# Kernel optimization log

Hardware: AMD Instinct MI355X
Metric: run time of the kernel (lower is better)

The kernel has to match this reference:

```python
import jax, jax.numpy as jnp
import numpy as np

N = 50000      # num_nodes
R = 32         # num_relations
H = 16         # hidden channels
C = 16         # num_classes
E = 1600000    # num_edges (avg degree 32)


def setup_inputs() -> dict:
    key = jax.random.key(0)
    ks = jax.random.split(key, 8)
    edge_index = jax.random.randint(ks[0], (2, E), 0, N)
    edge_type = jnp.sort(jax.random.randint(ks[1], (E,), 0, R))
    # per-relation [start, end) slices into the sorted edge list (is_sorted=True)
    starts = jnp.searchsorted(edge_type, jnp.arange(R))
    ends = jnp.searchsorted(edge_type, jnp.arange(R) + 1)
    tensor_slice = jnp.stack([starts, ends], axis=1)
    s = 0.05
    W1 = jax.random.normal(ks[2], (R, N, H), dtype=jnp.float32) * s   # layer-1 per-relation embedding (x=None)
    root1 = jax.random.normal(ks[3], (N, H), dtype=jnp.float32) * s  # root weight acts as embedding when x=None
    bias1 = jax.random.normal(ks[4], (H,), dtype=jnp.float32) * s
    W2 = jax.random.normal(ks[5], (R, H, C), dtype=jnp.float32) * s
    root2 = jax.random.normal(ks[6], (H, C), dtype=jnp.float32) * s
    bias2 = jax.random.normal(ks[7], (C,), dtype=jnp.float32) * s
    return {"edge_index": edge_index, "edge_type": edge_type, "tensor_slice": tensor_slice,
            "W1": W1, "root1": root1, "bias1": bias1,
            "W2": W2, "root2": root2, "bias2": bias2}


def reference(edge_index, edge_type, tensor_slice, W1, root1, bias1, W2, root2, bias2):
    src, dst = edge_index[0], edge_index[1]
    # ---- layer 1: x=None, so per-relation transform is an embedding lookup W1[r][src]
    msg1 = W1[edge_type, src]                                        # [E, H] relation-indexed gather
    h1 = root1 + jax.ops.segment_sum(msg1, dst, num_segments=N) + bias1
    h1 = jax.nn.relu(h1)
    # ---- layer 2: transform all nodes per relation once, then gather per edge
    t = jnp.einsum('nh,rhc->rnc', h1, W2)                            # [R, N, C]
    msg2 = t[edge_type, src]                                         # [E, C]
    h2 = h1 @ root2 + jax.ops.segment_sum(msg2, dst, num_segments=N) + bias2
    return jax.nn.log_softmax(h2, axis=1)
```

## Files before the change

### kernel.cpp

```cpp
#include <hip/hip_runtime.h>

static constexpr int H  = 16;
static constexpr int C  = 16;

__global__ void k1_scatter(const int* __restrict__ srcv, const int* __restrict__ dstv,
                           const int* __restrict__ etv, const float* __restrict__ W1,
                           float* __restrict__ acc1, int E, int N) {
    int t = blockIdx.x * blockDim.x + threadIdx.x;
    if (t >= E * 16) return;
    int e = t >> 4;
    int c = t & 15;
    int s = srcv[e];
    int d = dstv[e];
    int r = etv[e];
    float v = W1[((size_t)r * N + (size_t)s) * H + c];
    unsafeAtomicAdd(acc1 + (size_t)d * H + c, v);
}

__global__ void k2_fin1(const float* __restrict__ root1, const float* __restrict__ bias1,
                        const float* __restrict__ acc1, float* __restrict__ h1, int total4) {
    int i = blockIdx.x * blockDim.x + threadIdx.x;
    if (i >= total4) return;
    float4 rv = ((const float4*)root1)[i];
    float4 av = ((const float4*)acc1)[i];
    float4 bv = ((const float4*)bias1)[i & 3];
    float4 o;
    o.x = fmaxf(rv.x + av.x + bv.x, 0.0f);
    o.y = fmaxf(rv.y + av.y + bv.y, 0.0f);
    o.z = fmaxf(rv.z + av.z + bv.z, 0.0f);
    o.w = fmaxf(rv.w + av.w + bv.w, 0.0f);
    ((float4*)h1)[i] = o;
}

__global__ void k3_scatter(const int* __restrict__ srcv, const int* __restrict__ dstv,
                           const int* __restrict__ etv, const float* __restrict__ h1,
                           const float* __restrict__ W2, float* __restrict__ out, int E) {
    int t = blockIdx.x * blockDim.x + threadIdx.x;
    if (t >= E * 16) return;
    int e = t >> 4;
    int c = t & 15;
    int s = srcv[e];
    int d = dstv[e];
    int r = etv[e];
    const float4* hr = (const float4*)(h1 + (size_t)s * H);
    float4 h0 = hr[0], h1v = hr[1], h2v = hr[2], h3v = hr[3];
    const float* w = W2 + (size_t)r * H * C + c;
    float acc = 0.f;
    acc += h0.x * w[0 * C];  acc += h0.y * w[1 * C];
    acc += h0.z * w[2 * C];  acc += h0.w * w[3 * C];
    acc += h1v.x * w[4 * C]; acc += h1v.y * w[5 * C];
    acc += h1v.z * w[6 * C]; acc += h1v.w * w[7 * C];
    acc += h2v.x * w[8 * C]; acc += h2v.y * w[9 * C];
    acc += h2v.z * w[10 * C]; acc += h2v.w * w[11 * C];
    acc += h3v.x * w[12 * C]; acc += h3v.y * w[13 * C];
    acc += h3v.z * w[14 * C]; acc += h3v.w * w[15 * C];
    unsafeAtomicAdd(out + (size_t)d * C + c, acc);
}

__global__ void k4_fin2(const float* __restrict__ h1, const float* __restrict__ root2,
                        const float* __restrict__ bias2, float* __restrict__ out, int N) {
    int n = blockIdx.x * blockDim.x + threadIdx.x;
    if (n >= N) return;
    const float* hr = h1 + (size_t)n * H;
    float h[16];
#pragma unroll
    for (int k = 0; k < 16; ++k) h[k] = hr[k];
    float* o = out + (size_t)n * C;
    float z[16];
#pragma unroll
    for (int c = 0; c < 16; ++c) {
        float acc = o[c] + bias2[c];
#pragma unroll
        for (int k = 0; k < 16; ++k) acc += h[k] * root2[k * C + c];
        z[c] = acc;
    }
    float m = z[0];
#pragma unroll
    for (int c = 1; c < 16; ++c) m = fmaxf(m, z[c]);
    float se = 0.f;
#pragma unroll
    for (int c = 0; c < 16; ++c) se += __expf(z[c] - m);
    float lse = m + __logf(se);
#pragma unroll
    for (int c = 0; c < 16; ++c) o[c] = z[c] - lse;
}

extern "C" void kernel_launch(void* const* d_in, const int* in_sizes, int n_in,
                              void* d_out, int out_size, void* d_ws, size_t ws_size,
                              hipStream_t stream) {
    const int*   edge_index = (const int*)d_in[0];
    const int*   edge_type  = (const int*)d_in[1];
    const float* W1    = (const float*)d_in[3];
    const float* root1 = (const float*)d_in[4];
    const float* bias1 = (const float*)d_in[5];
    const float* W2    = (const float*)d_in[6];
    const float* root2 = (const float*)d_in[7];
    const float* bias2 = (const float*)d_in[8];
    float* out = (float*)d_out;

    const int E = in_sizes[0] / 2;
    const int N = in_sizes[4] / H;
    const int* srcv = edge_index;
    const int* dstv = edge_index + E;

    float* acc1 = (float*)d_ws;
    float* h1   = acc1 + (size_t)N * H;

    hipMemsetAsync(acc1, 0, (size_t)N * H * sizeof(float), stream);
    hipMemsetAsync(out, 0, (size_t)out_size * sizeof(float), stream);

    const int B = 256;
    int t16 = E * 16;
    k1_scatter<<<(t16 + B - 1) / B, B, 0, stream>>>(srcv, dstv, edge_type, W1, acc1, E, N);
    int total4 = N * H / 4;
    k2_fin1<<<(total4 + B - 1) / B, B, 0, stream>>>(root1, bias1, acc1, h1, total4);
    k3_scatter<<<(t16 + B - 1) / B, B, 0, stream>>>(srcv, dstv, edge_type, h1, W2, out, E);
    k4_fin2<<<(N + B - 1) / B, B, 0, stream>>>(h1, root2, bias2, out, N);
}
```

Baseline: 216.4 us.

## Compute layer-2 edge messages with bf16 MFMA over per-relation edge chunks

```diff
diff --git a/kernel.cpp b/kernel.cpp
--- a/kernel.cpp
+++ b/kernel.cpp
@@ -1,7 +1,16 @@
 #include <hip/hip_runtime.h>
+#include <hip/hip_bf16.h>
 
 static constexpr int H  = 16;
 static constexpr int C  = 16;
+
+typedef __attribute__((ext_vector_type(8))) short bf16x8;
+typedef __attribute__((ext_vector_type(4))) float f32x4;
+
+static __device__ inline unsigned short f2bf(float x) {
+    __hip_bfloat16 b = __float2bfloat16(x);
+    return *reinterpret_cast<unsigned short*>(&b);
+}
 
 __global__ void k1_scatter(const int* __restrict__ srcv, const int* __restrict__ dstv,
                            const int* __restrict__ etv, const float* __restrict__ W1,
@@ -18,7 +27,8 @@
 }
 
 __global__ void k2_fin1(const float* __restrict__ root1, const float* __restrict__ bias1,
-                        const float* __restrict__ acc1, float* __restrict__ h1, int total4) {
+                        const float* __restrict__ acc1, float* __restrict__ h1,
+                        unsigned int* __restrict__ h1bf , int total4) {
     int i = blockIdx.x * blockDim.x + threadIdx.x;
     if (i >= total4) return;
     float4 rv = ((const float4*)root1)[i];
@@ -30,31 +40,77 @@
     o.z = fmaxf(rv.z + av.z + bv.z, 0.0f);
     o.w = fmaxf(rv.w + av.w + bv.w, 0.0f);
     ((float4*)h1)[i] = o;
+    uint2 p;
+    p.x = ((unsigned)f2bf(o.y) << 16) | f2bf(o.x);
+    p.y = ((unsigned)f2bf(o.w) << 16) | f2bf(o.z);
+    ((uint2*)h1bf)[i] = p;
 }
 
-__global__ void k3_scatter(const int* __restrict__ srcv, const int* __restrict__ dstv,
-                           const int* __restrict__ etv, const float* __restrict__ h1,
-                           const float* __restrict__ W2, float* __restrict__ out, int E) {
-    int t = blockIdx.x * blockDim.x + threadIdx.x;
-    if (t >= E * 16) return;
-    int e = t >> 4;
-    int c = t & 15;
-    int s = srcv[e];
-    int d = dstv[e];
-    int r = etv[e];
-    const float4* hr = (const float4*)(h1 + (size_t)s * H);
-    float4 h0 = hr[0], h1v = hr[1], h2v = hr[2], h3v = hr[3];
-    const float* w = W2 + (size_t)r * H * C + c;
-    float acc = 0.f;
-    acc += h0.x * w[0 * C];  acc += h0.y * w[1 * C];
-    acc += h0.z * w[2 * C];  acc += h0.w * w[3 * C];
-    acc += h1v.x * w[4 * C]; acc += h1v.y * w[5 * C];
-    acc += h1v.z * w[6 * C]; acc += h1v.w * w[7 * C];
-    acc += h2v.x * w[8 * C]; acc += h2v.y * w[9 * C];
-    acc += h2v.z * w[10 * C]; acc += h2v.w * w[11 * C];
-    acc += h3v.x * w[12 * C]; acc += h3v.y * w[13 * C];
-    acc += h3v.z * w[14 * C]; acc += h3v.w * w[15 * C];
-    unsafeAtomicAdd(out + (size_t)d * C + c, acc);
+__global__ void k0_prep(const int* __restrict__ ts, int* __restrict__ chunk_off, int R) {
+    if (blockIdx.x == 0 && threadIdx.x == 0) {
+        int acc = 0;
+        for (int r = 0; r < R; ++r) {
+            chunk_off[r] = acc;
+            int cnt = ts[2 * r + 1] - ts[2 * r];
+            acc += (cnt + 15) >> 4;
+        }
+        chunk_off[R] = acc;
+    }
+}
+
+__global__ void k0_cast(const float* __restrict__ W2, unsigned short* __restrict__ w2t,
+                        int total ) {
+    int i = blockIdx.x * blockDim.x + threadIdx.x;
+    if (i >= total) return;
+    int r = i >> 8;
+    int kc = i & 255;
+    int k = kc >> 4;
+    int c = kc & 15;
+    w2t[(r << 8) + (c << 4) + k] = f2bf(W2[i]);
+}
+
+__global__ void k3_mfma(const int* __restrict__ srcv, const int* __restrict__ dstv,
+                        const int* __restrict__ ts, const int* __restrict__ chunk_off,
+                        const unsigned short* __restrict__ h1bf,
+                        const unsigned short* __restrict__ w2t,
+                        float* __restrict__ out, int R) {
+    int w = (blockIdx.x * blockDim.x + threadIdx.x) >> 6;
+    int l = threadIdx.x & 63;
+    int total = chunk_off[R];
+    if (w >= total) return;
+    int lo = 0, hi = R;
+    while (hi - lo > 1) {
+        int mid = (lo + hi) >> 1;
+        if (chunk_off[mid] <= w) lo = mid; else hi = mid;
+    }
+    int r = lo;
+    int e0 = ts[2 * r] + ((w - chunk_off[r]) << 4);
+    int eend = ts[2 * r + 1];
+    int n_e = min(16, eend - e0);
+
+    int rowA = l & 15;
+    int kg = l >> 4;
+    int eA = e0 + min(rowA, n_e - 1);
+    int s = srcv[eA];
+
+    bf16x8 a = {0, 0, 0, 0, 0, 0, 0, 0};
+    bf16x8 b = {0, 0, 0, 0, 0, 0, 0, 0};
+    if (kg < 2) {
+        a = *(const bf16x8*)(h1bf + ((size_t)s << 4) + (kg << 3));
+        b = *(const bf16x8*)(w2t + ((size_t)r << 8) + (rowA << 4) + (kg << 3));
+    }
+    f32x4 d = {0.f, 0.f, 0.f, 0.f};
+    d = __builtin_amdgcn_mfma_f32_16x16x32_bf16(a, b, d, 0, 0, 0);
+
+    int c = l & 15;
+#pragma unroll
+    for (int j = 0; j < 4; ++j) {
+        int row = (kg << 2) + j;
+        if (row < n_e) {
+            int dd = dstv[e0 + row];
+            unsafeAtomicAdd(out + ((size_t)dd << 4) + c, d[j]);
+        }
+    }
 }
 
 __global__ void k4_fin2(const float* __restrict__ h1, const float* __restrict__ root2,
@@ -88,8 +144,9 @@
 extern "C" void kernel_launch(void* const* d_in, const int* in_sizes, int n_in,
                               void* d_out, int out_size, void* d_ws, size_t ws_size,
                               hipStream_t stream) {
-    const int*   edge_index = (const int*)d_in[0];
-    const int*   edge_type  = (const int*)d_in[1];
+    const int*   edge_index   = (const int*)d_in[0];
+    const int*   edge_type    = (const int*)d_in[1];
+    const int*   tensor_slice = (const int*)d_in[2];
     const float* W1    = (const float*)d_in[3];
     const float* root1 = (const float*)d_in[4];
     const float* bias1 = (const float*)d_in[5];
@@ -100,20 +157,30 @@
 
     const int E = in_sizes[0] / 2;
     const int N = in_sizes[4] / H;
+    const int R = in_sizes[2] / 2;
     const int* srcv = edge_index;
     const int* dstv = edge_index + E;
 
     float* acc1 = (float*)d_ws;
     float* h1   = acc1 + (size_t)N * H;
+    unsigned short* h1bf = (unsigned short*)(h1 + (size_t)N * H);
+    unsigned short* w2t  = h1bf + (size_t)N * H;
+    int* chunk_off = (int*)(w2t + (size_t)R * H * C);
 
     hipMemsetAsync(acc1, 0, (size_t)N * H * sizeof(float), stream);
     hipMemsetAsync(out, 0, (size_t)out_size * sizeof(float), stream);
 
     const int B = 256;
+    k0_prep<<<1, 64, 0, stream>>>(tensor_slice, chunk_off, R);
+    k0_cast<<<(R * H * C + B - 1) / B, B, 0, stream>>>(W2, w2t, R * H * C);
     int t16 = E * 16;
     k1_scatter<<<(t16 + B - 1) / B, B, 0, stream>>>(srcv, dstv, edge_type, W1, acc1, E, N);
     int total4 = N * H / 4;
-    k2_fin1<<<(total4 + B - 1) / B, B, 0, stream>>>(root1, bias1, acc1, h1, total4);
-    k3_scatter<<<(t16 + B - 1) / B, B, 0, stream>>>(srcv, dstv, edge_type, h1, W2, out, E);
+    k2_fin1<<<(total4 + B - 1) / B, B, 0, stream>>>(root1, bias1, acc1, h1,
+                                                    (unsigned int*)h1bf, total4);
+    long long waves_ub = (long long)((E + 15) / 16) + R;
+    long long thr = waves_ub * 64;
+    k3_mfma<<<(int)((thr + B - 1) / B), B, 0, stream>>>(srcv, dstv, tensor_slice, chunk_off,
+                                                        h1bf, w2t, out, R);
     k4_fin2<<<(N + B - 1) / B, B, 0, stream>>>(h1, root2, bias2, out, N);
 }
```

Result: faster. 197.5 us (-8.7%).

## Bucket edges by destination block and aggregate in shared memory

Applied to the files above, without the earlier changes.

```diff
diff --git a/kernel.cpp b/kernel.cpp
--- a/kernel.cpp
+++ b/kernel.cpp
@@ -1,95 +1,172 @@
 #include <hip/hip_runtime.h>
-
-static constexpr int H  = 16;
-static constexpr int C  = 16;
-
-__global__ void k1_scatter(const int* __restrict__ srcv, const int* __restrict__ dstv,
-                           const int* __restrict__ etv, const float* __restrict__ W1,
-                           float* __restrict__ acc1, int E, int N) {
-    int t = blockIdx.x * blockDim.x + threadIdx.x;
-    if (t >= E * 16) return;
-    int e = t >> 4;
-    int c = t & 15;
-    int s = srcv[e];
-    int d = dstv[e];
-    int r = etv[e];
-    float v = W1[((size_t)r * N + (size_t)s) * H + c];
-    unsafeAtomicAdd(acc1 + (size_t)d * H + c, v);
-}
-
-__global__ void k2_fin1(const float* __restrict__ root1, const float* __restrict__ bias1,
-                        const float* __restrict__ acc1, float* __restrict__ h1, int total4) {
+#include <hip/hip_bf16.h>
+
+static constexpr int H = 16;
+static constexpr int C = 16;
+static constexpr int MAXNB = 4096;
+static constexpr int HIST_BLOCKS = 32;
+
+__global__ void k0_w2t(const float* __restrict__ W2, float* __restrict__ w2t, int total) {
     int i = blockIdx.x * blockDim.x + threadIdx.x;
-    if (i >= total4) return;
-    float4 rv = ((const float4*)root1)[i];
-    float4 av = ((const float4*)acc1)[i];
-    float4 bv = ((const float4*)bias1)[i & 3];
-    float4 o;
-    o.x = fmaxf(rv.x + av.x + bv.x, 0.0f);
-    o.y = fmaxf(rv.y + av.y + bv.y, 0.0f);
-    o.z = fmaxf(rv.z + av.z + bv.z, 0.0f);
-    o.w = fmaxf(rv.w + av.w + bv.w, 0.0f);
-    ((float4*)h1)[i] = o;
-}
-
-__global__ void k3_scatter(const int* __restrict__ srcv, const int* __restrict__ dstv,
-                           const int* __restrict__ etv, const float* __restrict__ h1,
-                           const float* __restrict__ W2, float* __restrict__ out, int E) {
-    int t = blockIdx.x * blockDim.x + threadIdx.x;
-    if (t >= E * 16) return;
-    int e = t >> 4;
-    int c = t & 15;
-    int s = srcv[e];
-    int d = dstv[e];
-    int r = etv[e];
-    const float4* hr = (const float4*)(h1 + (size_t)s * H);
-    float4 h0 = hr[0], h1v = hr[1], h2v = hr[2], h3v = hr[3];
-    const float* w = W2 + (size_t)r * H * C + c;
-    float acc = 0.f;
-    acc += h0.x * w[0 * C];  acc += h0.y * w[1 * C];
-    acc += h0.z * w[2 * C];  acc += h0.w * w[3 * C];
-    acc += h1v.x * w[4 * C]; acc += h1v.y * w[5 * C];
-    acc += h1v.z * w[6 * C]; acc += h1v.w * w[7 * C];
-    acc += h2v.x * w[8 * C]; acc += h2v.y * w[9 * C];
-    acc += h2v.z * w[10 * C]; acc += h2v.w * w[11 * C];
-    acc += h3v.x * w[12 * C]; acc += h3v.y * w[13 * C];
-    acc += h3v.z * w[14 * C]; acc += h3v.w * w[15 * C];
-    unsafeAtomicAdd(out + (size_t)d * C + c, acc);
-}
-
-__global__ void k4_fin2(const float* __restrict__ h1, const float* __restrict__ root2,
-                        const float* __restrict__ bias2, float* __restrict__ out, int N) {
-    int n = blockIdx.x * blockDim.x + threadIdx.x;
-    if (n >= N) return;
-    const float* hr = h1 + (size_t)n * H;
-    float h[16];
-#pragma unroll
-    for (int k = 0; k < 16; ++k) h[k] = hr[k];
-    float* o = out + (size_t)n * C;
-    float z[16];
-#pragma unroll
-    for (int c = 0; c < 16; ++c) {
-        float acc = o[c] + bias2[c];
-#pragma unroll
-        for (int k = 0; k < 16; ++k) acc += h[k] * root2[k * C + c];
-        z[c] = acc;
-    }
-    float m = z[0];
-#pragma unroll
-    for (int c = 1; c < 16; ++c) m = fmaxf(m, z[c]);
-    float se = 0.f;
-#pragma unroll
-    for (int c = 0; c < 16; ++c) se += __expf(z[c] - m);
-    float lse = m + __logf(se);
-#pragma unroll
-    for (int c = 0; c < 16; ++c) o[c] = z[c] - lse;
+    if (i >= total) return;
+    int r = i >> 8, kc = i & 255, k = kc >> 4, c = kc & 15;
+    w2t[(r << 8) + (c << 4) + k] = W2[i];
+}
+
+__global__ void kA_hist(const int* __restrict__ dstv, int* __restrict__ hist2d,
+                        int E, int NB) {
+    __shared__ int lh[MAXNB];
+    for (int i = threadIdx.x; i < NB; i += blockDim.x) lh[i] = 0;
+    __syncthreads();
+    int qtot = (E + 3) >> 2;
+    for (int q = blockIdx.x * blockDim.x + threadIdx.x; q < qtot;
+         q += gridDim.x * blockDim.x) {
+        int e0 = q << 2;
+        if (e0 + 4 <= E) {
+            int4 d = *(const int4*)(dstv + e0);
+            atomicAdd(&lh[d.x >> 4], 1);
+            atomicAdd(&lh[d.y >> 4], 1);
+            atomicAdd(&lh[d.z >> 4], 1);
+            atomicAdd(&lh[d.w >> 4], 1);
+        } else {
+            for (int e = e0; e < E; ++e) atomicAdd(&lh[dstv[e] >> 4], 1);
+        }
+    }
+    __syncthreads();
+    int* row = hist2d + (size_t)blockIdx.x * MAXNB;
+    for (int i = threadIdx.x; i < NB; i += blockDim.x) row[i] = lh[i];
+}
+
+__global__ void kB1_sum(const int* __restrict__ hist2d, int* __restrict__ cnt, int NB) {
+    int i = blockIdx.x * blockDim.x + threadIdx.x;
+    if (i >= NB) return;
+    int a = 0;
+#pragma unroll
+    for (int b = 0; b < HIST_BLOCKS; ++b) a += hist2d[(size_t)b * MAXNB + i];
+    cnt[i] = a;
+}
+
+__global__ void kB2_scan(const int* __restrict__ cnt, int* __restrict__ base,
+                         int* __restrict__ cursor, int NB) {
+    __shared__ int sh[1024];
+    int t = threadIdx.x;
+    int v[4]; int s = 0;
+#pragma unroll
+    for (int j = 0; j < 4; ++j) {
+        int idx = t * 4 + j;
+        v[j] = (idx < NB) ? cnt[idx] : 0;
+        s += v[j];
+    }
+    sh[t] = s;
+    __syncthreads();
+    for (int off = 1; off < 1024; off <<= 1) {
+        int val = (t >= off) ? sh[t - off] : 0;
+        __syncthreads();
+        sh[t] += val;
+        __syncthreads();
+    }
+    int excl = sh[t] - s;
+#pragma unroll
+    for (int j = 0; j < 4; ++j) {
+        int idx = t * 4 + j;
+        if (idx < NB) { base[idx] = excl; cursor[idx] = excl; excl += v[j]; }
+    }
+}
+
+__global__ void kC_fill(const int* __restrict__ srcv, const int* __restrict__ dstv,
+                        const int* __restrict__ etv, int* __restrict__ cursor,
+                        unsigned* __restrict__ recs, int E) {
+    int q = blockIdx.x * blockDim.x + threadIdx.x;
+    int e0 = q << 2;
+    if (e0 >= E) return;
+    if (e0 + 4 <= E) {
+        int4 s = *(const int4*)(srcv + e0);
+        int4 d = *(const int4*)(dstv + e0);
+        int4 r = *(const int4*)(etv + e0);
+        int p;
+        p = atomicAdd(&cursor[d.x >> 4], 1); recs[p] = ((unsigned)r.x << 20) | ((unsigned)s.x << 4) | (unsigned)(d.x & 15);
+        p = atomicAdd(&cursor[d.y >> 4], 1); recs[p] = ((unsigned)r.y << 20) | ((unsigned)s.y << 4) | (unsigned)(d.y & 15);
+        p = atomicAdd(&cursor[d.z >> 4], 1); recs[p] = ((unsigned)r.z << 20) | ((unsigned)s.z << 4) | (unsigned)(d.z & 15);
+        p = atomicAdd(&cursor[d.w >> 4], 1); recs[p] = ((unsigned)r.w << 20) | ((unsigned)s.w << 4) | (unsigned)(d.w & 15);
+    } else {
+        for (int e = e0; e < E; ++e) {
+            int p = atomicAdd(&cursor[dstv[e] >> 4], 1);
+            recs[p] = ((unsigned)etv[e] << 20) | ((unsigned)srcv[e] << 4) | (unsigned)(dstv[e] & 15);
+        }
+    }
+}
+
+__global__ void k1p(const unsigned* __restrict__ recs, const int* __restrict__ base,
+                    const int* __restrict__ cnt, const float* __restrict__ W1,
+                    const float* __restrict__ root1, const float* __restrict__ bias1,
+                    float* __restrict__ h1, int N) {
+    __shared__ float win[256];
+    int b = blockIdx.x;
+    win[threadIdx.x] = 0.f;
+    __syncthreads();
+    int st = base[b], n = cnt[b];
+    int g = threadIdx.x >> 4, c = threadIdx.x & 15;
+    for (int i = g; i < n; i += 16) {
+        unsigned rec = recs[st + i];
+        int et = rec >> 20;
+        int src = (rec >> 4) & 0xFFFF;
+        int dl = rec & 15;
+        float w = W1[(((size_t)et * N + src) << 4) + c];
+        atomicAdd(&win[(dl << 4) + c], w);
+    }
+    __syncthreads();
+    int d = (b << 4) + g;
+    if (d < N) {
+        float val = win[threadIdx.x] + root1[(d << 4) + c] + bias1[c];
+        h1[((size_t)d << 4) + c] = fmaxf(val, 0.f);
+    }
+}
+
+__global__ void k3p(const unsigned* __restrict__ recs, const int* __restrict__ base,
+                    const int* __restrict__ cnt, const float* __restrict__ h1,
+                    const float* __restrict__ w2t, const float* __restrict__ root2,
+                    const float* __restrict__ bias2, float* __restrict__ out, int N) {
+    __shared__ float win[256];
+    int b = blockIdx.x;
+    win[threadIdx.x] = 0.f;
+    __syncthreads();
+    int st = base[b], n = cnt[b];
+    int g = threadIdx.x >> 4, c = threadIdx.x & 15;
+    for (int i = g; i < n; i += 16) {
+        unsigned rec = recs[st + i];
+        int et = rec >> 20;
+        int src = (rec >> 4) & 0xFFFF;
+        int dl = rec & 15;
+        const float4* hp = (const float4*)(h1 + ((size_t)src << 4));
+        float4 h0 = hp[0], h1v = hp[1], h2v = hp[2], h3v = hp[3];
+        const float4* wp = (const float4*)(w2t + (et << 8) + (c << 4));
+        float4 w0 = wp[0], w1 = wp[1], w2v = wp[2], w3 = wp[3];
+        float acc = h0.x * w0.x + h0.y * w0.y + h0.z * w0.z + h0.w * w0.w
+                  + h1v.x * w1.x + h1v.y * w1.y + h1v.z * w1.z + h1v.w * w1.w
+                  + h2v.x * w2v.x + h2v.y * w2v.y + h2v.z * w2v.z + h2v.w * w2v.w
+                  + h3v.x * w3.x + h3v.y * w3.y + h3v.z * w3.z + h3v.w * w3.w;
+        atomicAdd(&win[(dl << 4) + c], acc);
+    }
+    __syncthreads();
+    int d = (b << 4) + g;
+    if (d >= N) return;
+    const float* hd = h1 + ((size_t)d << 4);
+    float z = win[threadIdx.x] + bias2[c];
+#pragma unroll
+    for (int k = 0; k < 16; ++k) z += hd[k] * root2[(k << 4) + c];
+    float m = z;
+#pragma unroll
+    for (int off = 8; off; off >>= 1) m = fmaxf(m, __shfl_xor(m, off, 16));
+    float ex = __expf(z - m), se = ex;
+#pragma unroll
+    for (int off = 8; off; off >>= 1) se += __shfl_xor(se, off, 16);
+    out[((size_t)d << 4) + c] = z - m - __logf(se);
 }
 
 extern "C" void kernel_launch(void* const* d_in, const int* in_sizes, int n_in,
                               void* d_out, int out_size, void* d_ws, size_t ws_size,
                               hipStream_t stream) {
     const int*   edge_index = (const int*)d_in[0];
-    const int*   edge_type  = (const int*)d_in[1];
     const float* W1    = (const float*)d_in[3];
     const float* root1 = (const float*)d_in[4];
     const float* bias1 = (const float*)d_in[5];
@@ -100,20 +177,28 @@
 
     const int E = in_sizes[0] / 2;
     const int N = in_sizes[4] / H;
+    const int R = in_sizes[2] / 2;
+    const int NB = (N + 15) >> 4;
     const int* srcv = edge_index;
     const int* dstv = edge_index + E;
-
-    float* acc1 = (float*)d_ws;
-    float* h1   = acc1 + (size_t)N * H;
-
-    hipMemsetAsync(acc1, 0, (size_t)N * H * sizeof(float), stream);
-    hipMemsetAsync(out, 0, (size_t)out_size * sizeof(float), stream);
+    const int* etv  = (const int*)d_in[1];
+
+    char* p = (char*)d_ws;
+    unsigned* recs = (unsigned*)p;        p += (size_t)E * 4;
+    float* h1 = (float*)p;                p += (size_t)N * 16 * 4;
+    float* w2t = (float*)p;               p += (size_t)R * 256 * 4;
+    int* hist2d = (int*)p;                p += (size_t)HIST_BLOCKS * MAXNB * 4;
+    int* cnt = (int*)p;                   p += (size_t)NB * 4;
+    int* base = (int*)p;                  p += (size_t)NB * 4;
+    int* cursor = (int*)p;
 
     const int B = 256;
-    int t16 = E * 16;
-    k1_scatter<<<(t16 + B - 1) / B, B, 0, stream>>>(srcv, dstv, edge_type, W1, acc1, E, N);
-    int total4 = N * H / 4;
-    k2_fin1<<<(total4 + B - 1) / B, B, 0, stream>>>(root1, bias1, acc1, h1, total4);
-    k3_scatter<<<(t16 + B - 1) / B, B, 0, stream>>>(srcv, dstv, edge_type, h1, W2, out, E);
-    k4_fin2<<<(N + B - 1) / B, B, 0, stream>>>(h1, root2, bias2, out, N);
-}
+    k0_w2t<<<(R * 256 + B - 1) / B, B, 0, stream>>>(W2, w2t, R * 256);
+    kA_hist<<<HIST_BLOCKS, B, 0, stream>>>(dstv, hist2d, E, NB);
+    kB1_sum<<<(NB + B - 1) / B, B, 0, stream>>>(hist2d, cnt, NB);
+    kB2_scan<<<1, 1024, 0, stream>>>(cnt, base, cursor, NB);
+    int qtot = (E + 3) / 4;
+    kC_fill<<<(qtot + B - 1) / B, B, 0, stream>>>(srcv, dstv, etv, cursor, recs, E);
+    k1p<<<NB, B, 0, stream>>>(recs, base, cnt, W1, root1, bias1, h1, N);
+    k3p<<<NB, B, 0, stream>>>(recs, base, cnt, h1, w2t, root2, bias2, out, N);
+}
```

Result: slower. 468.7 us (+116.6%).
